# Optimization experiments

Hardware: AMD Instinct MI355X
Metric: run time of the kernel (lower is better)

The kernel has to match this reference:

```python
import jax, jax.numpy as jnp
import numpy as np

NUM_NODES = 100000
NUM_EDGES = 1200000
DIM = 64
NUM_LAYERS = 3
NUM_GRAPHS = 512
BN_EPS = 1e-5


def setup_inputs() -> dict:
    key = jax.random.key(0)
    ks = jax.random.split(key, 12)
    x = jax.random.normal(ks[0], (NUM_NODES, DIM), dtype=jnp.float32)
    edge_index = jax.random.randint(ks[1], (2, NUM_EDGES), 0, NUM_NODES, dtype=jnp.int64)
    edge_weight = jax.random.uniform(ks[2], (NUM_EDGES,), dtype=jnp.float32)
    batch = jnp.sort(jax.random.randint(ks[3], (NUM_NODES,), 0, NUM_GRAPHS, dtype=jnp.int64))
    W1 = jax.random.normal(ks[4], (NUM_LAYERS, DIM, DIM), dtype=jnp.float32) * 0.1
    b1 = jax.random.normal(ks[5], (NUM_LAYERS, DIM), dtype=jnp.float32) * 0.1
    W2 = jax.random.normal(ks[6], (NUM_LAYERS, DIM, DIM), dtype=jnp.float32) * 0.1
    b2 = jax.random.normal(ks[7], (NUM_LAYERS, DIM), dtype=jnp.float32) * 0.1
    gamma = jax.random.uniform(ks[8], (NUM_LAYERS, DIM), dtype=jnp.float32) + 0.5
    beta = jax.random.normal(ks[9], (NUM_LAYERS, DIM), dtype=jnp.float32) * 0.1
    return {"x": x, "edge_index": edge_index, "edge_weight": edge_weight,
            "batch": batch, "pool": 0, "W1": W1, "b1": b1, "W2": W2,
            "b2": b2, "gamma": gamma, "beta": beta}


def reference(x, edge_index, edge_weight, batch, pool, W1, b1, W2, b2, gamma, beta):
    # WGINConv (eps=0): h = MLP(x + scatter_add(edge_weight * x[src] -> dst))
    # then ReLU, then BatchNorm1d in training mode (batch statistics).
    src, dst = edge_index[0], edge_index[1]
    n_nodes = x.shape[0]
    xs = []
    for i in range(W1.shape[0]):
        msg = x[src] * edge_weight[:, None]                       # [E, D] gather
        agg = jax.ops.segment_sum(msg, dst, num_segments=n_nodes)  # [N, D] scatter-add
        h = agg + x                                                # (1+eps)*x, eps=0
        h = jax.nn.relu(h @ W1[i].T + b1[i]) @ W2[i].T + b2[i]     # GIN MLP
        h = jax.nn.relu(h)
        mu = h.mean(0)
        var = ((h - mu) ** 2).mean(0)                              # biased var (BN train)
        x = gamma[i] * (h - mu) * jax.lax.rsqrt(var + BN_EPS) + beta[i]
        xs.append(x)
    if pool == 0:  # 'add' pooling (static python int)
        xpool = [jax.ops.segment_sum(v, batch, num_segments=NUM_GRAPHS) for v in xs]
    else:          # 'mean' pooling
        counts = jax.ops.segment_sum(jnp.ones((n_nodes,), x.dtype), batch,
                                     num_segments=NUM_GRAPHS)
        denom = jnp.maximum(counts, 1.0)[:, None]
        xpool = [jax.ops.segment_sum(v, batch, num_segments=NUM_GRAPHS) / denom for v in xs]
    return (jnp.concatenate(xpool, axis=1), jnp.concatenate(xs, axis=1))
```

## Files before the change

kernel.cpp:

```cpp
#include <hip/hip_runtime.h>

#define N_NODES 100000
#define N_EDGES 1200000
#define DIM     64
#define N_LAYERS 3
#define N_GRAPHS 512
#define OUTD    192
#define BN_EPS  1e-5f

#define NPB 64
#define LDS_PITCH 65
#define NLBLK ((N_NODES + NPB - 1) / NPB)

#define BSHIFT 9
#define BUCK_NODES (1 << BSHIFT)
#define NBUK ((N_NODES + BUCK_NODES - 1) / BUCK_NODES)
#define EPB 4096
#define NPBLK ((N_EDGES + EPB - 1) / EPB)

__device__ __forceinline__ unsigned short f2bf(float f) {
    unsigned u = __float_as_uint(f);
    return (unsigned short)((u + 0x7FFFu + ((u >> 16) & 1u)) >> 16);
}
__device__ __forceinline__ float bf2f(unsigned short h) {
    return __uint_as_float(((unsigned)h) << 16);
}

__global__ void transpose_w(const float* __restrict__ W1, const float* __restrict__ W2,
                            float* __restrict__ W1T, float* __restrict__ W2T,
                            float* __restrict__ idaff, int* __restrict__ tot) {
    int idx = blockIdx.x * blockDim.x + threadIdx.x;
    if (idx < 128) idaff[idx] = (idx < 64) ? 1.0f : 0.0f;
    if (idx < NBUK + 4) tot[idx] = 0;
    if (idx >= N_LAYERS * DIM * DIM) return;
    int l = idx >> 12;
    int r = idx & 4095;
    int j = r >> 6;
    int k = r & 63;
    int dstp = (l << 12) + k * DIM + j;
    W1T[dstp] = W1[idx];
    W2T[dstp] = W2[idx];
}

__global__ void __launch_bounds__(256) part_hist(const int* __restrict__ dst,
                                                 int* __restrict__ hist,
                                                 int* __restrict__ tot) {
    __shared__ int h[NBUK];
    int t = threadIdx.x;
    if (t < NBUK) h[t] = 0;
    __syncthreads();
    int base = blockIdx.x * EPB;
    for (int i = t; i < EPB; i += 256) {
        int e = base + i;
        if (e < N_EDGES) atomicAdd(&h[dst[e] >> BSHIFT], 1);
    }
    __syncthreads();
    if (t < NBUK) {
        int v = h[t];
        hist[blockIdx.x * NBUK + t] = v;
        if (v) atomicAdd(&tot[t], v);
    }
}

__global__ void __launch_bounds__(256) base_fill(const int* __restrict__ hist,
                                                 const int* __restrict__ tot,
                                                 int* __restrict__ base) {
    __shared__ int c[512];
    __shared__ int ssum[256];
    __shared__ int btot[256];
    int b = blockIdx.x, t = threadIdx.x;
    btot[t] = (t < NBUK) ? tot[t] : 0;
    __syncthreads();
    for (int o = 1; o < 256; o <<= 1) {
        int add = (t >= o) ? btot[t - o] : 0;
        __syncthreads();
        btot[t] += add;
        __syncthreads();
    }
    int bstart_b = (b == 0) ? 0 : btot[b - 1];
    c[t] = (t < NPBLK) ? hist[t * NBUK + b] : 0;
    c[t + 256] = (t + 256 < NPBLK) ? hist[(t + 256) * NBUK + b] : 0;
    __syncthreads();
    int c0 = c[2 * t], c1 = c[2 * t + 1];
    int ps = c0 + c1;
    ssum[t] = ps;
    __syncthreads();
    int v = ps;
    for (int o = 1; o < 256; o <<= 1) {
        int add = (t >= o) ? ssum[t - o] : 0;
        __syncthreads();
        ssum[t] += add;
        __syncthreads();
    }
    int excl = ssum[t] - v + bstart_b;
    if (2 * t < NPBLK)     base[(2 * t) * NBUK + b] = excl;
    if (2 * t + 1 < NPBLK) base[(2 * t + 1) * NBUK + b] = excl + c0;
}

__global__ void __launch_bounds__(256) part_scatter(
        const int* __restrict__ src, const int* __restrict__ dst,
        const float* __restrict__ ew, const int* __restrict__ base,
        int2* __restrict__ pp) {
    __shared__ int cur[NBUK];
    int t = threadIdx.x;
    if (t < NBUK) cur[t] = base[blockIdx.x * NBUK + t];
    __syncthreads();
    int bb = blockIdx.x * EPB;
    for (int i = t; i < EPB; i += 256) {
        int e = bb + i;
        if (e < N_EDGES) {
            int d = dst[e];
            int bk = d >> BSHIFT;
            int pos = atomicAdd(&cur[bk], 1);
            int dl = d & (BUCK_NODES - 1);
            pp[pos] = make_int2(src[e] | (dl << 17), __float_as_int(ew[e]));
        }
    }
}

__global__ void __launch_bounds__(256) csr_build(
        const int2* __restrict__ pp, const int* __restrict__ tot,
        int* __restrict__ seg, int2* __restrict__ pe) {
    __shared__ int cnt[BUCK_NODES];
    __shared__ int ssum[256];
    __shared__ int btot[256];
    int b = blockIdx.x, t = threadIdx.x;
    btot[t] = (t < NBUK) ? tot[t] : 0;
    __syncthreads();
    for (int o = 1; o < 256; o <<= 1) {
        int add = (t >= o) ? btot[t - o] : 0;
        __syncthreads();
        btot[t] += add;
        __syncthreads();
    }
    int eend = btot[b];
    int ebeg = (b == 0) ? 0 : btot[b - 1];
    cnt[t] = 0;
    cnt[t + 256] = 0;
    __syncthreads();
    for (int e = ebeg + t; e < eend; e += 256)
        atomicAdd(&cnt[pp[e].x >> 17], 1);
    __syncthreads();
    int c0 = cnt[2 * t], c1 = cnt[2 * t + 1];
    int ps = c0 + c1;
    ssum[t] = ps;
    __syncthreads();
    int v = ps;
    for (int o = 1; o < 256; o <<= 1) {
        int add = (t >= o) ? ssum[t - o] : 0;
        __syncthreads();
        ssum[t] += add;
        __syncthreads();
    }
    int excl = ssum[t] - v;
    int o0 = ebeg + excl;
    int o1 = o0 + c0;
    int n0 = (b << BSHIFT) + 2 * t;
    if (n0 < N_NODES) seg[n0] = o0;
    if (n0 + 1 < N_NODES) seg[n0 + 1] = o1;
    __syncthreads();
    cnt[2 * t] = o0;
    cnt[2 * t + 1] = o1;
    __syncthreads();
    for (int e = ebeg + t; e < eend; e += 256) {
        int2 p = pp[e];
        int pos = atomicAdd(&cnt[p.x >> 17], 1);
        pe[pos] = make_int2(p.x & 0x1FFFF, p.y);
    }
    if (b == 0 && t == 0) seg[N_NODES] = N_EDGES;
}

template <int BF16IN>
__global__ void __launch_bounds__(256) layer_kernel(
    const float* __restrict__ x_in, int xstride,
    const unsigned short* __restrict__ x16in,
    unsigned short* __restrict__ x16out, int wr16,
    const int* __restrict__ seg,
    const int2* __restrict__ pe,
    const float* __restrict__ affine ,
    const float* __restrict__ W1T, const float* __restrict__ b1,
    const float* __restrict__ W2T, const float* __restrict__ b2,
    float* __restrict__ out ,
    float* __restrict__ pstat ) {
    __shared__ float lds[NPB * LDS_PITCH];
    int t = threadIdx.x;
    int lane = t & 63;
    int wid = __builtin_amdgcn_readfirstlane(t >> 6);
    int nbase = blockIdx.x * NPB;

    int slot = lane >> 4;
    int col  = lane & 15;
    const float4* aff4 = (const float4*)affine;
    float4 sc4 = aff4[col];
    float4 sh4 = aff4[16 + col];

    for (int nn = 0; nn < 16; ++nn) {
        int nl = wid * 16 + nn;
        int n = nbase + nl;
        float ax = 0.f, ay = 0.f, az = 0.f, aw = 0.f, wsa = 0.f;
        float bx = 0.f, by = 0.f, bz = 0.f, bw = 0.f, wsb = 0.f;
        if (n < N_NODES) {
            int beg = seg[n];
            int end = seg[n + 1];
#define GBODY(EI, X, Y, Z, W, WS)                                              \
            if ((EI) < end) {                                                  \
                int2 p = pe[EI];                                               \
                float w = __int_as_float(p.y);                                 \
                float vx, vy, vz, vw;                                          \
                if (BF16IN) {                                                  \
                    ushort4 hv =                                               \
                        ((const ushort4*)(x16in + (size_t)p.x * DIM))[col];    \
                    vx = bf2f(hv.x); vy = bf2f(hv.y);                          \
                    vz = bf2f(hv.z); vw = bf2f(hv.w);                          \
                } else {                                                       \
                    float4 fv =                                                \
                        ((const float4*)(x_in + (size_t)p.x * xstride))[col];  \
                    vx = fv.x; vy = fv.y; vz = fv.z; vw = fv.w;                \
                }                                                              \
                X = fmaf(w, vx, X); Y = fmaf(w, vy, Y);                        \
                Z = fmaf(w, vz, Z); W = fmaf(w, vw, W);                        \
                WS += w;                                                       \
            }
            for (int e = beg; e < end; e += 16) {
                int e0 = e + slot;
                GBODY(e0,      ax, ay, az, aw, wsa)
                GBODY(e0 + 4,  bx, by, bz, bw, wsb)
                GBODY(e0 + 8,  ax, ay, az, aw, wsa)
                GBODY(e0 + 12, bx, by, bz, bw, wsb)
            }
#undef GBODY
        }
        float sx = ax + bx, sy = ay + by, sz = az + bz, sw = aw + bw;
        float ws = wsa + wsb;
        sx += __shfl_xor(sx, 16); sy += __shfl_xor(sy, 16);
        sz += __shfl_xor(sz, 16); sw += __shfl_xor(sw, 16);
        ws += __shfl_xor(ws, 16);
        sx += __shfl_xor(sx, 32); sy += __shfl_xor(sy, 32);
        sz += __shfl_xor(sz, 32); sw += __shfl_xor(sw, 32);
        ws += __shfl_xor(ws, 32);
        if (lane < 16) {
            float r0 = 0.f, r1 = 0.f, r2 = 0.f, r3 = 0.f;
            if (n < N_NODES) {
                const float4* xr =
                    (const float4*)(x_in + (size_t)n * xstride) + col;
                float4 s = *xr;
                float shw = 1.0f + ws;
                r0 = fmaf(sc4.x, sx + s.x, sh4.x * shw);
                r1 = fmaf(sc4.y, sy + s.y, sh4.y * shw);
                r2 = fmaf(sc4.z, sz + s.z, sh4.z * shw);
                r3 = fmaf(sc4.w, sw + s.w, sh4.w * shw);
            }
            int lb = nl * LDS_PITCH + col * 4;
            lds[lb] = r0; lds[lb + 1] = r1; lds[lb + 2] = r2; lds[lb + 3] = r3;
        }
    }
    __syncthreads();

    float h[16];
#pragma unroll
    for (int jj = 0; jj < 16; ++jj) h[jj] = b1[wid * 16 + jj];
#pragma unroll 4
    for (int k = 0; k < DIM; ++k) {
        float xv = lds[lane * LDS_PITCH + k];
        const float* wr = W1T + k * DIM + wid * 16;
#pragma unroll
        for (int jj = 0; jj < 16; ++jj) h[jj] = fmaf(xv, wr[jj], h[jj]);
    }
#pragma unroll
    for (int jj = 0; jj < 16; ++jj) h[jj] = fmaxf(h[jj], 0.0f);
    __syncthreads();
#pragma unroll
    for (int jj = 0; jj < 16; ++jj) lds[lane * LDS_PITCH + wid * 16 + jj] = h[jj];
    __syncthreads();

    float o[16];
#pragma unroll
    for (int jj = 0; jj < 16; ++jj) o[jj] = b2[wid * 16 + jj];
#pragma unroll 4
    for (int k = 0; k < DIM; ++k) {
        float hv = lds[lane * LDS_PITCH + k];
        const float* wr = W2T + k * DIM + wid * 16;
#pragma unroll
        for (int jj = 0; jj < 16; ++jj) o[jj] = fmaf(hv, wr[jj], o[jj]);
    }
    int n = nbase + lane;
    bool valid = (n < N_NODES);
#pragma unroll
    for (int jj = 0; jj < 16; ++jj) o[jj] = fmaxf(o[jj], 0.0f);
    if (valid) {
        float* orow = out + (size_t)n * OUTD + wid * 16;
#pragma unroll
        for (int jj = 0; jj < 16; jj += 4) {
            *(float4*)(orow + jj) = make_float4(o[jj], o[jj + 1], o[jj + 2], o[jj + 3]);
        }
        if (wr16) {
            unsigned short* hrow = x16out + (size_t)n * DIM + wid * 16;
#pragma unroll
            for (int jj = 0; jj < 16; jj += 4) {
                ushort4 hq;
                hq.x = f2bf(o[jj]);     hq.y = f2bf(o[jj + 1]);
                hq.z = f2bf(o[jj + 2]); hq.w = f2bf(o[jj + 3]);
                *(ushort4*)(hrow + jj) = hq;
            }
        }
    }

    float my_s = 0.0f, my_q = 0.0f;
#pragma unroll
    for (int jj = 0; jj < 16; ++jj) {
        float v = valid ? o[jj] : 0.0f;
        float vs = v, vq = v * v;
#pragma unroll
        for (int m = 1; m < 64; m <<= 1) {
            vs += __shfl_xor(vs, m);
            vq += __shfl_xor(vq, m);
        }
        if (lane == jj) { my_s = vs; my_q = vq; }
    }
    if (lane < 16) {
        size_t base = (size_t)blockIdx.x * 128 + wid * 16 + lane;
        pstat[base] = my_s;
        pstat[base + 64] = my_q;
    }
}

__global__ void __launch_bounds__(256) reduce_stats(
    const float* __restrict__ pstat,
    const float* __restrict__ gamma, const float* __restrict__ beta,
    float* __restrict__ ss ,
    float* __restrict__ pooled, int zpool) {
    __shared__ double part[16][16];
    int b = blockIdx.x;
    int t = threadIdx.x;
    if (zpool) {
        for (int i = b * 256 + t; i < N_GRAPHS * OUTD; i += 8 * 256)
            pooled[i] = 0.0f;
    }
    int slot = t & 15;
    int g = t >> 4;
    int d = b * 8 + (slot & 7);
    int off = (slot < 8) ? 0 : 64;
    double s = 0.0;
    for (int blk = g; blk < NLBLK; blk += 16)
        s += (double)pstat[(size_t)blk * 128 + off + d];
    part[g][slot] = s;
    __syncthreads();
    if (t < 16) {
        double x = 0.0;
#pragma unroll
        for (int k = 0; k < 16; ++k) x += part[k][t];
        part[0][t] = x;
    }
    __syncthreads();
    if (t < 8) {
        int dd = b * 8 + t;
        double mu = part[0][t] / (double)N_NODES;
        double var = part[0][8 + t] / (double)N_NODES - mu * mu;
        float inv = (float)(1.0 / sqrt(var + (double)BN_EPS));
        float sc = gamma[dd] * inv;
        ss[dd] = sc;
        ss[64 + dd] = beta[dd] - (float)mu * sc;
    }
}

__global__ void bn_pool(float* __restrict__ xs,
                        const int* __restrict__ batch,
                        const float* __restrict__ ss ,
                        float* __restrict__ pooled) {
    int g = blockIdx.x;
    int part = blockIdx.y;
    int d = threadIdx.x;
    int l = d >> 6, dd = d & 63;
    float sc = ss[l * 128 + dd];
    float sh = ss[l * 128 + 64 + dd];
    int start, end;
    {
        int lo = 0, hi = N_NODES;
        while (lo < hi) { int m = (lo + hi) >> 1; if (batch[m] < g) lo = m + 1; else hi = m; }
        start = lo;
    }
    {
        int lo = start, hi = N_NODES;
        while (lo < hi) { int m = (lo + hi) >> 1; if (batch[m] <= g) lo = m + 1; else hi = m; }
        end = lo;
    }
    float acc = 0.0f;
    for (int n = start + part; n < end; n += 4) {
        float* p = xs + (size_t)n * OUTD + d;
        float v = fmaf(*p, sc, sh);
        *p = v;
        acc += v;
    }
    atomicAdd(&pooled[(size_t)g * OUTD + d], acc);
}

extern "C" void kernel_launch(void* const* d_in, const int* in_sizes, int n_in,
                              void* d_out, int out_size, void* d_ws, size_t ws_size,
                              hipStream_t stream) {
    const float* x0    = (const float*)d_in[0];
    const int*   ei    = (const int*)d_in[1];
    const float* ew    = (const float*)d_in[2];
    const int*   batch = (const int*)d_in[3];
    const float* W1    = (const float*)d_in[5];
    const float* b1    = (const float*)d_in[6];
    const float* W2    = (const float*)d_in[7];
    const float* b2    = (const float*)d_in[8];
    const float* gamma = (const float*)d_in[9];
    const float* beta  = (const float*)d_in[10];

    float* pooled = (float*)d_out;
    float* xs     = pooled + (size_t)N_GRAPHS * OUTD;

    const int* src = ei;
    const int* dst = ei + N_EDGES;

    int2*  pe     = (int2*)d_ws;
    int*   seg    = (int*)(pe + N_EDGES);
    int*   tot    = seg + N_NODES + 4;
    float* W1T    = (float*)(tot + NBUK + 4);
    float* W2T    = W1T + N_LAYERS * DIM * DIM;
    float* idaff  = W2T + N_LAYERS * DIM * DIM;
    float* ss     = idaff + 128;
    float* pstat  = ss + N_LAYERS * 128;
    char* uni = (char*)(pstat + (size_t)NLBLK * 128);
    int2*  pp     = (int2*)uni;
    int*   hist   = (int*)(pp + N_EDGES);
    int*   pbase  = hist + (size_t)NPBLK * NBUK;
    unsigned short* x16a = (unsigned short*)uni;
    unsigned short* x16b = x16a + (size_t)N_NODES * DIM;

    transpose_w<<<(N_LAYERS * DIM * DIM + 255) / 256, 256, 0, stream>>>(
        W1, W2, W1T, W2T, idaff, tot);

    part_hist<<<NPBLK, 256, 0, stream>>>(dst, hist, tot);
    base_fill<<<NBUK, 256, 0, stream>>>(hist, tot, pbase);
    part_scatter<<<NPBLK, 256, 0, stream>>>(src, dst, ew, pbase, pp);
    csr_build<<<NBUK, 256, 0, stream>>>(pp, tot, seg, pe);

    for (int i = 0; i < N_LAYERS; ++i) {
        const float* xin = (i == 0) ? x0 : (xs + (size_t)(i - 1) * DIM);
        int xstride = (i == 0) ? DIM : OUTD;
        const float* affine = (i == 0) ? idaff : (ss + (size_t)(i - 1) * 128);
        const unsigned short* x16in = (i == 1) ? x16b : x16a;
        unsigned short* x16out = (i == 0) ? x16b : x16a;
        int wr16 = (i < N_LAYERS - 1) ? 1 : 0;

        if (i == 0) {
            layer_kernel<0><<<NLBLK, 256, 0, stream>>>(
                xin, xstride, x16in, x16out, wr16, seg, pe, affine,
                W1T + (size_t)i * DIM * DIM, b1 + (size_t)i * DIM,
                W2T + (size_t)i * DIM * DIM, b2 + (size_t)i * DIM,
                xs + (size_t)i * DIM, pstat);
        } else {
            layer_kernel<1><<<NLBLK, 256, 0, stream>>>(
                xin, xstride, x16in, x16out, wr16, seg, pe, affine,
                W1T + (size_t)i * DIM * DIM, b1 + (size_t)i * DIM,
                W2T + (size_t)i * DIM * DIM, b2 + (size_t)i * DIM,
                xs + (size_t)i * DIM, pstat);
        }

        reduce_stats<<<8, 256, 0, stream>>>(
            pstat, gamma + (size_t)i * DIM, beta + (size_t)i * DIM,
            ss + (size_t)i * 128, pooled, (i == N_LAYERS - 1) ? 1 : 0);
    }

    dim3 pgrid(N_GRAPHS, 4);
    bn_pool<<<pgrid, OUTD, 0, stream>>>(xs, batch, ss, pooled);
}
```

Baseline: 528.1 us.

## Fuse preprocessing kernels and replace BN stat reduction with atomics

```diff
diff --git a/kernel.cpp b/kernel.cpp
--- a/kernel.cpp
+++ b/kernel.cpp
@@ -26,106 +26,93 @@
     return __uint_as_float(((unsigned)h) << 16);
 }
 
-__global__ void transpose_w(const float* __restrict__ W1, const float* __restrict__ W2,
-                            float* __restrict__ W1T, float* __restrict__ W2T,
-                            float* __restrict__ idaff, int* __restrict__ tot) {
-    int idx = blockIdx.x * blockDim.x + threadIdx.x;
-    if (idx < 128) idaff[idx] = (idx < 64) ? 1.0f : 0.0f;
-    if (idx < NBUK + 4) tot[idx] = 0;
-    if (idx >= N_LAYERS * DIM * DIM) return;
-    int l = idx >> 12;
-    int r = idx & 4095;
-    int j = r >> 6;
-    int k = r & 63;
-    int dstp = (l << 12) + k * DIM + j;
-    W1T[dstp] = W1[idx];
-    W2T[dstp] = W2[idx];
-}
-
-__global__ void __launch_bounds__(256) part_hist(const int* __restrict__ dst,
-                                                 int* __restrict__ hist,
-                                                 int* __restrict__ tot) {
+__global__ void __launch_bounds__(256) prep_hist(
+        const float* __restrict__ W1, const float* __restrict__ W2,
+        const int* __restrict__ dst,
+        float* __restrict__ W1T, float* __restrict__ W2T,
+        int* __restrict__ hist, float* __restrict__ accum,
+        float* __restrict__ pooled) {
     __shared__ int h[NBUK];
-    int t = threadIdx.x;
+    int k = blockIdx.x, t = threadIdx.x;
+    int gid = k * 256 + t;
+    if (gid < N_LAYERS * DIM * DIM) {
+        int l = gid >> 12;
+        int r = gid & 4095;
+        int j = r >> 6;
+        int kk = r & 63;
+        int dstp = (l << 12) + kk * DIM + j;
+        W1T[dstp] = W1[gid];
+        W2T[dstp] = W2[gid];
+    }
+    if (k == 48) {
+        for (int i = t; i < N_LAYERS * 128; i += 256) accum[i] = 0.0f;
+    }
+    if (k >= 49) {
+        for (int i = (k - 49) * 256 + t; i < N_GRAPHS * OUTD; i += 244 * 256)
+            pooled[i] = 0.0f;
+    }
     if (t < NBUK) h[t] = 0;
     __syncthreads();
-    int base = blockIdx.x * EPB;
-    for (int i = t; i < EPB; i += 256) {
-        int e = base + i;
-        if (e < N_EDGES) atomicAdd(&h[dst[e] >> BSHIFT], 1);
-    }
-    __syncthreads();
+    int e0 = k * EPB;
+    int e1 = e0 + EPB; if (e1 > N_EDGES) e1 = N_EDGES;
+    for (int e = e0 + t; e < e1; e += 256) atomicAdd(&h[dst[e] >> BSHIFT], 1);
+    __syncthreads();
+    if (t < NBUK) hist[k * NBUK + t] = h[t];
+}
+
+__global__ void __launch_bounds__(256) part_scatter2(
+        const int* __restrict__ src, const int* __restrict__ dst,
+        const float* __restrict__ ew, const int* __restrict__ hist,
+        int2* __restrict__ pp) {
+    __shared__ int ps[256];
+    __shared__ int cur[NBUK];
+    int k = blockIdx.x, t = threadIdx.x;
+    int full = 0, pre = 0;
     if (t < NBUK) {
-        int v = h[t];
-        hist[blockIdx.x * NBUK + t] = v;
-        if (v) atomicAdd(&tot[t], v);
-    }
-}
-
-__global__ void __launch_bounds__(256) base_fill(const int* __restrict__ hist,
-                                                 const int* __restrict__ tot,
-                                                 int* __restrict__ base) {
-    __shared__ int c[512];
-    __shared__ int ssum[256];
-    __shared__ int btot[256];
-    int b = blockIdx.x, t = threadIdx.x;
-    btot[t] = (t < NBUK) ? tot[t] : 0;
-    __syncthreads();
+#pragma unroll 8
+        for (int r = 0; r < NPBLK; ++r) {
+            int hv = hist[r * NBUK + t];
+            full += hv;
+            pre += (r < k) ? hv : 0;
+        }
+    }
+    ps[t] = (t < NBUK) ? full : 0;
+    __syncthreads();
+    int v = ps[t];
     for (int o = 1; o < 256; o <<= 1) {
-        int add = (t >= o) ? btot[t - o] : 0;
-        __syncthreads();
-        btot[t] += add;
-        __syncthreads();
-    }
-    int bstart_b = (b == 0) ? 0 : btot[b - 1];
-    c[t] = (t < NPBLK) ? hist[t * NBUK + b] : 0;
-    c[t + 256] = (t + 256 < NPBLK) ? hist[(t + 256) * NBUK + b] : 0;
-    __syncthreads();
-    int c0 = c[2 * t], c1 = c[2 * t + 1];
-    int ps = c0 + c1;
-    ssum[t] = ps;
-    __syncthreads();
-    int v = ps;
-    for (int o = 1; o < 256; o <<= 1) {
-        int add = (t >= o) ? ssum[t - o] : 0;
-        __syncthreads();
-        ssum[t] += add;
-        __syncthreads();
-    }
-    int excl = ssum[t] - v + bstart_b;
-    if (2 * t < NPBLK)     base[(2 * t) * NBUK + b] = excl;
-    if (2 * t + 1 < NPBLK) base[(2 * t + 1) * NBUK + b] = excl + c0;
-}
-
-__global__ void __launch_bounds__(256) part_scatter(
-        const int* __restrict__ src, const int* __restrict__ dst,
-        const float* __restrict__ ew, const int* __restrict__ base,
-        int2* __restrict__ pp) {
-    __shared__ int cur[NBUK];
-    int t = threadIdx.x;
-    if (t < NBUK) cur[t] = base[blockIdx.x * NBUK + t];
-    __syncthreads();
-    int bb = blockIdx.x * EPB;
+        int add = (t >= o) ? ps[t - o] : 0;
+        __syncthreads();
+        ps[t] += add;
+        __syncthreads();
+    }
+    if (t < NBUK) cur[t] = (ps[t] - v) + pre;
+    __syncthreads();
+    int bb = k * EPB;
     for (int i = t; i < EPB; i += 256) {
         int e = bb + i;
         if (e < N_EDGES) {
             int d = dst[e];
             int bk = d >> BSHIFT;
             int pos = atomicAdd(&cur[bk], 1);
-            int dl = d & (BUCK_NODES - 1);
-            pp[pos] = make_int2(src[e] | (dl << 17), __float_as_int(ew[e]));
-        }
-    }
-}
-
-__global__ void __launch_bounds__(256) csr_build(
-        const int2* __restrict__ pp, const int* __restrict__ tot,
+            pp[pos] = make_int2(src[e] | ((d & (BUCK_NODES - 1)) << 17),
+                                __float_as_int(ew[e]));
+        }
+    }
+}
+
+__global__ void __launch_bounds__(256) csr_build2(
+        const int2* __restrict__ pp, const int* __restrict__ hist,
         int* __restrict__ seg, int2* __restrict__ pe) {
     __shared__ int cnt[BUCK_NODES];
     __shared__ int ssum[256];
     __shared__ int btot[256];
     int b = blockIdx.x, t = threadIdx.x;
-    btot[t] = (t < NBUK) ? tot[t] : 0;
+    int full = 0;
+    if (t < NBUK) {
+#pragma unroll 8
+        for (int r = 0; r < NPBLK; ++r) full += hist[r * NBUK + t];
+    }
+    btot[t] = (t < NBUK) ? full : 0;
     __syncthreads();
     for (int o = 1; o < 256; o <<= 1) {
         int add = (t >= o) ? btot[t - o] : 0;
@@ -177,12 +164,14 @@
     unsigned short* __restrict__ x16out, int wr16,
     const int* __restrict__ seg,
     const int2* __restrict__ pe,
-    const float* __restrict__ affine ,
+    const float* __restrict__ accumPrev,
+    const float* __restrict__ gprev, const float* __restrict__ bprev,
     const float* __restrict__ W1T, const float* __restrict__ b1,
     const float* __restrict__ W2T, const float* __restrict__ b2,
     float* __restrict__ out ,
-    float* __restrict__ pstat ) {
+    float* __restrict__ accumCur ) {
     __shared__ float lds[NPB * LDS_PITCH];
+    __shared__ float aff[128];
     int t = threadIdx.x;
     int lane = t & 63;
     int wid = __builtin_amdgcn_readfirstlane(t >> 6);
@@ -190,9 +179,26 @@
 
     int slot = lane >> 4;
     int col  = lane & 15;
-    const float4* aff4 = (const float4*)affine;
-    float4 sc4 = aff4[col];
-    float4 sh4 = aff4[16 + col];
+
+    if (BF16IN) {
+        if (t < 64) {
+            float s = accumPrev[t], q = accumPrev[64 + t];
+            float mu = s * (1.0f / N_NODES);
+            float var = q * (1.0f / N_NODES) - mu * mu;
+            float inv = 1.0f / sqrtf(var + BN_EPS);
+            float sc = gprev[t] * inv;
+            aff[t] = sc;
+            aff[64 + t] = bprev[t] - mu * sc;
+        }
+        __syncthreads();
+    }
+    float4 sc4, sh4;
+    if (BF16IN) {
+        sc4 = make_float4(aff[col * 4], aff[col * 4 + 1],
+                          aff[col * 4 + 2], aff[col * 4 + 3]);
+        sh4 = make_float4(aff[64 + col * 4], aff[64 + col * 4 + 1],
+                          aff[64 + col * 4 + 2], aff[64 + col * 4 + 3]);
+    }
 
     for (int nn = 0; nn < 16; ++nn) {
         int nl = wid * 16 + nn;
@@ -244,11 +250,16 @@
                 const float4* xr =
                     (const float4*)(x_in + (size_t)n * xstride) + col;
                 float4 s = *xr;
-                float shw = 1.0f + ws;
-                r0 = fmaf(sc4.x, sx + s.x, sh4.x * shw);
-                r1 = fmaf(sc4.y, sy + s.y, sh4.y * shw);
-                r2 = fmaf(sc4.z, sz + s.z, sh4.z * shw);
-                r3 = fmaf(sc4.w, sw + s.w, sh4.w * shw);
+                if (BF16IN) {
+                    float shw = 1.0f + ws;
+                    r0 = fmaf(sc4.x, sx + s.x, sh4.x * shw);
+                    r1 = fmaf(sc4.y, sy + s.y, sh4.y * shw);
+                    r2 = fmaf(sc4.z, sz + s.z, sh4.z * shw);
+                    r3 = fmaf(sc4.w, sw + s.w, sh4.w * shw);
+                } else {
+                    r0 = sx + s.x; r1 = sy + s.y;
+                    r2 = sz + s.z; r3 = sw + s.w;
+                }
             }
             int lb = nl * LDS_PITCH + col * 4;
             lds[lb] = r0; lds[lb + 1] = r1; lds[lb + 2] = r2; lds[lb + 3] = r3;
@@ -318,61 +329,28 @@
         if (lane == jj) { my_s = vs; my_q = vq; }
     }
     if (lane < 16) {
-        size_t base = (size_t)blockIdx.x * 128 + wid * 16 + lane;
-        pstat[base] = my_s;
-        pstat[base + 64] = my_q;
-    }
-}
-
-__global__ void __launch_bounds__(256) reduce_stats(
-    const float* __restrict__ pstat,
-    const float* __restrict__ gamma, const float* __restrict__ beta,
-    float* __restrict__ ss ,
-    float* __restrict__ pooled, int zpool) {
-    __shared__ double part[16][16];
-    int b = blockIdx.x;
-    int t = threadIdx.x;
-    if (zpool) {
-        for (int i = b * 256 + t; i < N_GRAPHS * OUTD; i += 8 * 256)
-            pooled[i] = 0.0f;
-    }
-    int slot = t & 15;
-    int g = t >> 4;
-    int d = b * 8 + (slot & 7);
-    int off = (slot < 8) ? 0 : 64;
-    double s = 0.0;
-    for (int blk = g; blk < NLBLK; blk += 16)
-        s += (double)pstat[(size_t)blk * 128 + off + d];
-    part[g][slot] = s;
-    __syncthreads();
-    if (t < 16) {
-        double x = 0.0;
-#pragma unroll
-        for (int k = 0; k < 16; ++k) x += part[k][t];
-        part[0][t] = x;
-    }
-    __syncthreads();
-    if (t < 8) {
-        int dd = b * 8 + t;
-        double mu = part[0][t] / (double)N_NODES;
-        double var = part[0][8 + t] / (double)N_NODES - mu * mu;
-        float inv = (float)(1.0 / sqrt(var + (double)BN_EPS));
-        float sc = gamma[dd] * inv;
-        ss[dd] = sc;
-        ss[64 + dd] = beta[dd] - (float)mu * sc;
+        atomicAdd(&accumCur[wid * 16 + lane], my_s);
+        atomicAdd(&accumCur[64 + wid * 16 + lane], my_q);
     }
 }
 
 __global__ void bn_pool(float* __restrict__ xs,
                         const int* __restrict__ batch,
-                        const float* __restrict__ ss ,
+                        const float* __restrict__ accum ,
+                        const float* __restrict__ gamma ,
+                        const float* __restrict__ beta  ,
                         float* __restrict__ pooled) {
     int g = blockIdx.x;
     int part = blockIdx.y;
     int d = threadIdx.x;
     int l = d >> 6, dd = d & 63;
-    float sc = ss[l * 128 + dd];
-    float sh = ss[l * 128 + 64 + dd];
+    float s = accum[l * 128 + dd];
+    float q = accum[l * 128 + 64 + dd];
+    float mu = s * (1.0f / N_NODES);
+    float var = q * (1.0f / N_NODES) - mu * mu;
+    float inv = 1.0f / sqrtf(var + BN_EPS);
+    float sc = gamma[l * 64 + dd] * inv;
+    float sh = beta[l * 64 + dd] - mu * sc;
     int start, end;
     {
         int lo = 0, hi = N_NODES;
@@ -416,54 +394,45 @@
 
     int2*  pe     = (int2*)d_ws;
     int*   seg    = (int*)(pe + N_EDGES);
-    int*   tot    = seg + N_NODES + 4;
-    float* W1T    = (float*)(tot + NBUK + 4);
+    float* W1T    = (float*)(seg + N_NODES + 4);
     float* W2T    = W1T + N_LAYERS * DIM * DIM;
-    float* idaff  = W2T + N_LAYERS * DIM * DIM;
-    float* ss     = idaff + 128;
-    float* pstat  = ss + N_LAYERS * 128;
-    char* uni = (char*)(pstat + (size_t)NLBLK * 128);
+    float* accum  = W2T + N_LAYERS * DIM * DIM;
+    char* uni = (char*)(accum + N_LAYERS * 128 + 16);
     int2*  pp     = (int2*)uni;
     int*   hist   = (int*)(pp + N_EDGES);
-    int*   pbase  = hist + (size_t)NPBLK * NBUK;
     unsigned short* x16a = (unsigned short*)uni;
     unsigned short* x16b = x16a + (size_t)N_NODES * DIM;
 
-    transpose_w<<<(N_LAYERS * DIM * DIM + 255) / 256, 256, 0, stream>>>(
-        W1, W2, W1T, W2T, idaff, tot);
-
-    part_hist<<<NPBLK, 256, 0, stream>>>(dst, hist, tot);
-    base_fill<<<NBUK, 256, 0, stream>>>(hist, tot, pbase);
-    part_scatter<<<NPBLK, 256, 0, stream>>>(src, dst, ew, pbase, pp);
-    csr_build<<<NBUK, 256, 0, stream>>>(pp, tot, seg, pe);
+    prep_hist<<<NPBLK, 256, 0, stream>>>(W1, W2, dst, W1T, W2T, hist,
+                                         accum, pooled);
+    part_scatter2<<<NPBLK, 256, 0, stream>>>(src, dst, ew, hist, pp);
+    csr_build2<<<NBUK, 256, 0, stream>>>(pp, hist, seg, pe);
 
     for (int i = 0; i < N_LAYERS; ++i) {
         const float* xin = (i == 0) ? x0 : (xs + (size_t)(i - 1) * DIM);
         int xstride = (i == 0) ? DIM : OUTD;
-        const float* affine = (i == 0) ? idaff : (ss + (size_t)(i - 1) * 128);
         const unsigned short* x16in = (i == 1) ? x16b : x16a;
         unsigned short* x16out = (i == 0) ? x16b : x16a;
         int wr16 = (i < N_LAYERS - 1) ? 1 : 0;
+        const float* accumPrev = accum + (size_t)(i - 1) * 128;
+        float* accumCur = accum + (size_t)i * 128;
 
         if (i == 0) {
             layer_kernel<0><<<NLBLK, 256, 0, stream>>>(
-                xin, xstride, x16in, x16out, wr16, seg, pe, affine,
+                xin, xstride, x16in, x16out, wr16, seg, pe,
+                accum, gamma, beta,
+                W1T, b1, W2T, b2, xs, accumCur);
+        } else {
+            layer_kernel<1><<<NLBLK, 256, 0, stream>>>(
+                xin, xstride, x16in, x16out, wr16, seg, pe,
+                accumPrev, gamma + (size_t)(i - 1) * DIM,
+                beta + (size_t)(i - 1) * DIM,
                 W1T + (size_t)i * DIM * DIM, b1 + (size_t)i * DIM,
                 W2T + (size_t)i * DIM * DIM, b2 + (size_t)i * DIM,
-                xs + (size_t)i * DIM, pstat);
-        } else {
-            layer_kernel<1><<<NLBLK, 256, 0, stream>>>(
-                xin, xstride, x16in, x16out, wr16, seg, pe, affine,
-                W1T + (size_t)i * DIM * DIM, b1 + (size_t)i * DIM,
-                W2T + (size_t)i * DIM * DIM, b2 + (size_t)i * DIM,
-                xs + (size_t)i * DIM, pstat);
-        }
-
-        reduce_stats<<<8, 256, 0, stream>>>(
-            pstat, gamma + (size_t)i * DIM, beta + (size_t)i * DIM,
-            ss + (size_t)i * 128, pooled, (i == N_LAYERS - 1) ? 1 : 0);
+                xs + (size_t)i * DIM, accumCur);
+        }
     }
 
     dim3 pgrid(N_GRAPHS, 4);
-    bn_pool<<<pgrid, OUTD, 0, stream>>>(xs, batch, ss, pooled);
-}
+    bn_pool<<<pgrid, OUTD, 0, stream>>>(xs, batch, accum, gamma, beta, pooled);
+}
```

Measured after the change: 636.0 us. 20.4% more time.
